# Kernel tuning notes

Hardware: AMD Instinct MI355X
Metric: run time of the kernel (lower is better)

Reference implementation:

```python
import jax, jax.numpy as jnp
import numpy as np
from itertools import combinations

DIM = 7
EPS = 1e-4

# --- static exterior-derivative index maps (mirrors _build_derivative_maps d2_map) ---
_IDX3 = list(combinations(range(DIM), 3))           # 35 ordered 3-form multi-indices
_POS2 = {t: i for i, t in enumerate(combinations(range(DIM), 2))}  # 21 2-form positions
_d2 = []
for _out, (i, j, k) in enumerate(_IDX3):
    for _p, (a, b, c) in enumerate([(i, j, k), (j, i, k), (k, i, j)]):
        bc = tuple(sorted((b, c)))
        s = (-1) ** _p * (1 if (b, c) == bc else -1)
        _d2.append((_out, _POS2[bc], a, s))
OUT_POS = np.array([t[0] for t in _d2], dtype=np.int32)   # (105,)
IN_POS  = np.array([t[1] for t in _d2], dtype=np.int32)   # (105,)
DCOORD  = np.array([t[2] for t in _d2], dtype=np.int32)   # (105,)
SIGNS   = np.array([t[3] for t in _d2], dtype=np.float32) # (105,)


def setup_inputs() -> dict:
    key = jax.random.key(0)
    k1, k2, k3 = jax.random.split(key, 3)
    B = 262144
    x = jax.random.normal(k1, (B, DIM), dtype=jnp.float32)
    W1 = jax.random.normal(k2, (DIM, 32), dtype=jnp.float32) * 0.3
    W2 = jax.random.normal(k3, (32, 21), dtype=jnp.float32) * 0.3
    return {"x": x, "W1": W1, "W2": W2}


def reference(x, W1, W2):
    """ExteriorDerivative.apply_2form_fd with omega_fn(x) = sin(x @ W1) @ W2.

    x: (B, 7) -> d_omega: (B, 35)
    """
    def omega_fn(xx):  # (..., 7) -> (..., 21)
        return jnp.sin(xx @ W1) @ W2

    B = x.shape[0]
    # All 7 +/- coordinate perturbations at once: (7, B, 7)
    pert = EPS * jnp.eye(DIM, dtype=x.dtype)[:, None, :]
    omega_plus = omega_fn(x[None] + pert)    # (7, B, 21)
    omega_minus = omega_fn(x[None] - pert)   # (7, B, 21)
    fd = (omega_plus - omega_minus) / (2.0 * EPS)  # central differences (7, B, 21)

    # Gather the 105 (deriv_coord, in_pos) derivative values -> (105, B)
    grads = fd[DCOORD, :, IN_POS]
    contrib = jnp.asarray(SIGNS)[:, None] * grads  # (105, B)

    # Scatter-add into the 35 3-form components (duplicate out positions accumulate)
    d_omega = jnp.zeros((B, 35), dtype=x.dtype).at[:, OUT_POS].add(contrib.T)
    return d_omega
```

## Files before the change

### kernel.cpp

```cpp
#include <hip/hip_runtime.h>

#define DIM 7
#define HD  32
#define P2  21
#define P3  35
#define BLK 256
#define NT  3
#define TPW 4
#define WPB (BLK / 64)
#define WSLAB (TPW * 16 * DIM)

typedef __attribute__((ext_vector_type(8))) _Float16 half8v;
typedef __attribute__((ext_vector_type(4))) float  float4v;

static __device__ const int TI[P3] = {
  0,0,0,0,0,0,0,0,0,0,0,0,0,0,0,
  1,1,1,1,1,1,1,1,1,1,
  2,2,2,2,2,2,
  3,3,3,
  4};
static __device__ const int TJ[P3] = {
  1,1,1,1,1, 2,2,2,2, 3,3,3, 4,4, 5,
  2,2,2,2, 3,3,3, 4,4, 5,
  3,3,3, 4,4, 5,
  4,4, 5,
  5};
static __device__ const int TK[P3] = {
  2,3,4,5,6, 3,4,5,6, 4,5,6, 5,6, 6,
  3,4,5,6, 4,5,6, 5,6, 6,
  4,5,6, 5,6, 6,
  5,6, 6,
  6};

__device__ __forceinline__ int pos2(int a, int b) {
  return a * 6 - (a * (a - 1)) / 2 + (b - a - 1);
}

__global__ __launch_bounds__(BLK)
void dform_kernel(const float* __restrict__ x,
                  const float* __restrict__ W1,
                  const float* __restrict__ W2,
                  float* __restrict__ out, int B)
{
  __shared__ _Float16 Mh[NT * 16 * HD];
  __shared__ float xs[WPB * WSLAB];

  const int tid  = threadIdx.x;
  const int lane = tid & 63;
  const int wid  = tid >> 6;
  const int lrow = lane & 15;
  const int lgrp = lane >> 4;

  for (int idx = tid; idx < NT * 16 * HD; idx += BLK) {
    int col = idx >> 5;
    int h   = idx & (HD - 1);
    float val = 0.f;
    if (col < P3) {
      int i = TI[col], j = TJ[col], k = TK[col];
      val = W1[i * HD + h] * W2[h * P2 + pos2(j, k)]
          - W1[j * HD + h] * W2[h * P2 + pos2(i, k)]
          + W1[k * HD + h] * W2[h * P2 + pos2(i, j)];
    }
    Mh[idx] = (_Float16)val;
  }

  const int h0 = lgrp * 8;
  float w1r[DIM][8];
  #pragma unroll
  for (int j = 0; j < DIM; ++j) {
    float4 p0 = *reinterpret_cast<const float4*>(&W1[j * HD + h0]);
    float4 p1 = *reinterpret_cast<const float4*>(&W1[j * HD + h0 + 4]);
    w1r[j][0] = p0.x; w1r[j][1] = p0.y; w1r[j][2] = p0.z; w1r[j][3] = p0.w;
    w1r[j][4] = p1.x; w1r[j][5] = p1.y; w1r[j][6] = p1.z; w1r[j][7] = p1.w;
  }

  const int gw = blockIdx.x * WPB + wid;
  const int tb = gw * TPW;
  const long long xbase = (long long)gw * WSLAB;
  float* xw = xs + wid * WSLAB;
  if (xbase + WSLAB <= (long long)B * DIM) {
    const float4* src = reinterpret_cast<const float4*>(x + xbase);
    float4* dst = reinterpret_cast<float4*>(xw);
    dst[lane] = src[lane];
    if (lane < WSLAB / 4 - 64) dst[lane + 64] = src[lane + 64];
  } else {
    for (int i = lane; i < WSLAB; i += 64) {
      long long g = xbase + i;
      xw[i] = (g < (long long)B * DIM) ? x[g] : 0.f;
    }
  }

  __syncthreads();

  half8v mfrag[NT];
  #pragma unroll
  for (int c = 0; c < NT; ++c) {
    int off = (c * 16 + lrow) * HD + h0;
    mfrag[c] = *reinterpret_cast<const half8v*>(&Mh[off]);
  }

  float xr[TPW][DIM];
  #pragma unroll
  for (int i = 0; i < TPW; ++i)
    #pragma unroll
    for (int j = 0; j < DIM; ++j)
      xr[i][j] = xw[(i * 16 + lrow) * DIM + j];

  #pragma unroll
  for (int i = 0; i < TPW; ++i) {
    const int t = tb + i;
    if (t * 16 >= B) break;

    half8v cfrag;
    #pragma unroll
    for (int e = 0; e < 8; ++e) {
      float tv = 0.f;
      #pragma unroll
      for (int j = 0; j < DIM; ++j) tv = fmaf(xr[i][j], w1r[j][e], tv);
      cfrag[e] = (_Float16)__cosf(tv);
    }

    float4v acc[NT];
    #pragma unroll
    for (int c = 0; c < NT; ++c) {
      acc[c][0] = 0.f; acc[c][1] = 0.f; acc[c][2] = 0.f; acc[c][3] = 0.f;
      acc[c] = __builtin_amdgcn_mfma_f32_16x16x32_f16(mfrag[c], cfrag, acc[c], 0, 0, 0);
    }

    const int row = t * 16 + lrow;
    if (row < B) {
      float* op = out + (long long)row * P3;
      const int cb = lgrp * 4;
      *reinterpret_cast<float4*>(op + cb) =
          make_float4(acc[0][0], acc[0][1], acc[0][2], acc[0][3]);
      *reinterpret_cast<float4*>(op + 16 + cb) =
          make_float4(acc[1][0], acc[1][1], acc[1][2], acc[1][3]);
      if (lgrp == 0) {
        *reinterpret_cast<float2*>(op + 32) = make_float2(acc[2][0], acc[2][1]);
        op[34] = acc[2][2];
      }
    }
  }
}

extern "C" void kernel_launch(void* const* d_in, const int* in_sizes, int n_in,
                              void* d_out, int out_size, void* d_ws, size_t ws_size,
                              hipStream_t stream) {
  const float* x  = (const float*)d_in[0];
  const float* W1 = (const float*)d_in[1];
  const float* W2 = (const float*)d_in[2];
  float* out = (float*)d_out;
  const int B = in_sizes[0] / DIM;
  const int ntiles = (B + 15) / 16;
  const int waves  = (ntiles + TPW - 1) / TPW;
  const int grid   = (waves + WPB - 1) / WPB;
  hipLaunchKernelGGL(dform_kernel, dim3(grid), dim3(BLK), 0, stream,
                     x, W1, W2, out, B);
}
```

Measured before the change: 19.49 us.

## Precompute M in a separate kernel and stage output tiles through LDS

The fused weight matrix M is now built once by a single-block pre-kernel into workspace instead of being rebuilt redundantly in every block. This removes per-block W2 gathers and the block-wide __syncthreads. Output rows are staged per wave in LDS and written as contiguous float4 runs, replacing strided 35-float row stores. This adds a second kernel launch and extra LDS traffic with wave barriers.

```diff
diff --git a/kernel.cpp b/kernel.cpp
--- a/kernel.cpp
+++ b/kernel.cpp
@@ -9,6 +9,7 @@
 #define TPW 4
 #define WPB (BLK / 64)
 #define WSLAB (TPW * 16 * DIM)
+#define OBUF  (16 * P3)
 
 typedef __attribute__((ext_vector_type(8))) _Float16 half8v;
 typedef __attribute__((ext_vector_type(4))) float  float4v;
@@ -36,22 +37,11 @@
   return a * 6 - (a * (a - 1)) / 2 + (b - a - 1);
 }
 
-__global__ __launch_bounds__(BLK)
-void dform_kernel(const float* __restrict__ x,
-                  const float* __restrict__ W1,
-                  const float* __restrict__ W2,
-                  float* __restrict__ out, int B)
+__global__ void build_m(const float* __restrict__ W1,
+                        const float* __restrict__ W2,
+                        _Float16* __restrict__ mws)
 {
-  __shared__ _Float16 Mh[NT * 16 * HD];
-  __shared__ float xs[WPB * WSLAB];
-
-  const int tid  = threadIdx.x;
-  const int lane = tid & 63;
-  const int wid  = tid >> 6;
-  const int lrow = lane & 15;
-  const int lgrp = lane >> 4;
-
-  for (int idx = tid; idx < NT * 16 * HD; idx += BLK) {
+  for (int idx = threadIdx.x; idx < NT * 16 * HD; idx += BLK) {
     int col = idx >> 5;
     int h   = idx & (HD - 1);
     float val = 0.f;
@@ -61,23 +51,30 @@
           - W1[j * HD + h] * W2[h * P2 + pos2(i, k)]
           + W1[k * HD + h] * W2[h * P2 + pos2(i, j)];
     }
-    Mh[idx] = (_Float16)val;
+    mws[idx] = (_Float16)val;
   }
+}
 
-  const int h0 = lgrp * 8;
-  float w1r[DIM][8];
-  #pragma unroll
-  for (int j = 0; j < DIM; ++j) {
-    float4 p0 = *reinterpret_cast<const float4*>(&W1[j * HD + h0]);
-    float4 p1 = *reinterpret_cast<const float4*>(&W1[j * HD + h0 + 4]);
-    w1r[j][0] = p0.x; w1r[j][1] = p0.y; w1r[j][2] = p0.z; w1r[j][3] = p0.w;
-    w1r[j][4] = p1.x; w1r[j][5] = p1.y; w1r[j][6] = p1.z; w1r[j][7] = p1.w;
-  }
+__global__ __launch_bounds__(BLK)
+void dform_kernel(const float* __restrict__ x,
+                  const float* __restrict__ W1,
+                  const _Float16* __restrict__ mws,
+                  float* __restrict__ out, int B)
+{
+  __shared__ float ls[WPB][OBUF];
+
+  const int tid  = threadIdx.x;
+  const int lane = tid & 63;
+  const int wid  = tid >> 6;
+  const int lrow = lane & 15;
+  const int lgrp = lane >> 4;
+  const int h0   = lgrp * 8;
+
+  float* xw = &ls[wid][0];
 
   const int gw = blockIdx.x * WPB + wid;
   const int tb = gw * TPW;
   const long long xbase = (long long)gw * WSLAB;
-  float* xw = xs + wid * WSLAB;
   if (xbase + WSLAB <= (long long)B * DIM) {
     const float4* src = reinterpret_cast<const float4*>(x + xbase);
     float4* dst = reinterpret_cast<float4*>(xw);
@@ -90,21 +87,30 @@
     }
   }
 
-  __syncthreads();
+  float w1r[DIM][8];
+  #pragma unroll
+  for (int j = 0; j < DIM; ++j) {
+    float4 p0 = *reinterpret_cast<const float4*>(&W1[j * HD + h0]);
+    float4 p1 = *reinterpret_cast<const float4*>(&W1[j * HD + h0 + 4]);
+    w1r[j][0] = p0.x; w1r[j][1] = p0.y; w1r[j][2] = p0.z; w1r[j][3] = p0.w;
+    w1r[j][4] = p1.x; w1r[j][5] = p1.y; w1r[j][6] = p1.z; w1r[j][7] = p1.w;
+  }
 
   half8v mfrag[NT];
   #pragma unroll
-  for (int c = 0; c < NT; ++c) {
-    int off = (c * 16 + lrow) * HD + h0;
-    mfrag[c] = *reinterpret_cast<const half8v*>(&Mh[off]);
-  }
+  for (int c = 0; c < NT; ++c)
+    mfrag[c] = *reinterpret_cast<const half8v*>(&mws[(c * 16 + lrow) * HD + h0]);
 
+  __builtin_amdgcn_wave_barrier();
   float xr[TPW][DIM];
   #pragma unroll
   for (int i = 0; i < TPW; ++i)
     #pragma unroll
     for (int j = 0; j < DIM; ++j)
       xr[i][j] = xw[(i * 16 + lrow) * DIM + j];
+  __builtin_amdgcn_wave_barrier();
+
+  float* ob = &ls[wid][0];
 
   #pragma unroll
   for (int i = 0; i < TPW; ++i) {
@@ -127,19 +133,33 @@
       acc[c] = __builtin_amdgcn_mfma_f32_16x16x32_f16(mfrag[c], cfrag, acc[c], 0, 0, 0);
     }
 
-    const int row = t * 16 + lrow;
-    if (row < B) {
-      float* op = out + (long long)row * P3;
+    {
+      float* rp = ob + lrow * P3;
       const int cb = lgrp * 4;
-      *reinterpret_cast<float4*>(op + cb) =
+      *reinterpret_cast<float4*>(rp + cb) =
           make_float4(acc[0][0], acc[0][1], acc[0][2], acc[0][3]);
-      *reinterpret_cast<float4*>(op + 16 + cb) =
+      *reinterpret_cast<float4*>(rp + 16 + cb) =
           make_float4(acc[1][0], acc[1][1], acc[1][2], acc[1][3]);
       if (lgrp == 0) {
-        *reinterpret_cast<float2*>(op + 32) = make_float2(acc[2][0], acc[2][1]);
-        op[34] = acc[2][2];
+        *reinterpret_cast<float2*>(rp + 32) = make_float2(acc[2][0], acc[2][1]);
+        rp[34] = acc[2][2];
       }
     }
+    __builtin_amdgcn_wave_barrier();
+
+    if ((long long)(t + 1) * 16 <= B) {
+      float4* dst = reinterpret_cast<float4*>(out + (long long)t * OBUF);
+      const float4* src = reinterpret_cast<const float4*>(ob);
+      dst[lane]      = src[lane];
+      dst[lane + 64] = src[lane + 64];
+      if (lane < OBUF / 4 - 128) dst[lane + 128] = src[lane + 128];
+    } else {
+      long long base = (long long)t * OBUF;
+      long long lim  = (long long)B * P3;
+      for (int q = lane; q < OBUF; q += 64)
+        if (base + q < lim) out[base + q] = ob[q];
+    }
+    __builtin_amdgcn_wave_barrier();
   }
 }
 
@@ -150,10 +170,12 @@
   const float* W1 = (const float*)d_in[1];
   const float* W2 = (const float*)d_in[2];
   float* out = (float*)d_out;
+  _Float16* mws = (_Float16*)d_ws;
   const int B = in_sizes[0] / DIM;
   const int ntiles = (B + 15) / 16;
   const int waves  = (ntiles + TPW - 1) / TPW;
   const int grid   = (waves + WPB - 1) / WPB;
+  hipLaunchKernelGGL(build_m, dim3(1), dim3(BLK), 0, stream, W1, W2, mws);
   hipLaunchKernelGGL(dform_kernel, dim3(grid), dim3(BLK), 0, stream,
-                     x, W1, W2, out, B);
+                     x, W1, mws, out, B);
 }
```

Measured after the change: 20.87 us. 7.1% more time.
